# Optimization experiments

Hardware: AMD Instinct MI355X
Metric: run time of the kernel (lower is better)

The kernel has to match this reference:

```python
import jax, jax.numpy as jnp
import numpy as np

B, S, D, U = 32, 2048, 1024, 1024


def setup_inputs() -> dict:
    key = jax.random.key(0)
    ks = jax.random.split(key, 8)
    scale_in = 1.0 / np.sqrt(D)
    scale_u = 1.0 / np.sqrt(U)
    return {
        "query": jax.random.normal(ks[0], (B, D), dtype=jnp.float32),
        "values": jax.random.normal(ks[1], (B, S, D), dtype=jnp.float32),
        "W1": jax.random.normal(ks[2], (D, U), dtype=jnp.float32) * scale_in,
        "b1": jnp.zeros((U,), dtype=jnp.float32),
        "W2": jax.random.normal(ks[3], (D, U), dtype=jnp.float32) * scale_in,
        "b2": jnp.zeros((U,), dtype=jnp.float32),
        "V": jax.random.normal(ks[4], (U, 1), dtype=jnp.float32) * scale_u,
        "bV": jnp.zeros((1,), dtype=jnp.float32),
    }


def reference(query, values, W1, b1, W2, b2, V, bV):
    # values: [B, S, D] -> [B, S, U]; query: [B, D] -> [B, 1, U]
    proj_v = jnp.einsum("bsd,du->bsu", values, W1) + b1
    proj_q = (query @ W2 + b2)[:, None, :]
    # score: [B, S, 1]
    score = jnp.einsum("bsu,uo->bso", jnp.tanh(proj_v + proj_q), V) + bV
    attention_weights = jax.nn.softmax(score, axis=1)
    # context: [B, D]
    context_vector = jnp.sum(attention_weights * values, axis=1)
    return (context_vector, attention_weights)
```

## Files before the change

kernel.cpp:

```cpp
#include <hip/hip_runtime.h>

#define DEVFN __device__ __forceinline__
#define GLOBAL_AS __attribute__((address_space(1)))
#define LDS_AS __attribute__((address_space(3)))

typedef __attribute__((ext_vector_type(4))) float f32x4;
typedef __attribute__((ext_vector_type(8))) short short8;
typedef __attribute__((ext_vector_type(8))) unsigned short ushort8;

constexpr int CB = 32;
constexpr int CS = 2048;
constexpr int CD = 1024;
constexpr int CU = 1024;
constexpr int CM = CB * CS;

DEVFN unsigned f2bf_u(float f) {
    unsigned u = __float_as_uint(f);
    return (u + 0x7FFFu + ((u >> 16) & 1u)) >> 16;
}
DEVFN unsigned f2bf_pack(float lo, float hi) {
    return f2bf_u(lo) | (f2bf_u(hi) << 16);
}
DEVFN float tanh_fast(float x) {
    float e = exp2f(x * 2.885390081777927f);
    return 1.0f - 2.0f * __builtin_amdgcn_rcpf(e + 1.0f);
}

__global__ void k_bias1(const float* __restrict__ q, const float* __restrict__ W2,
                        float* __restrict__ bpart) {
    int dc = blockIdx.x, b = blockIdx.y;
    int t = threadIdx.x;
    __shared__ float qs[128];
    if (t < 128) qs[t] = q[b * CD + dc * 128 + t];
    __syncthreads();
    float acc0 = 0.f, acc1 = 0.f, acc2 = 0.f, acc3 = 0.f;
    const float* w2 = W2 + (size_t)(dc * 128) * CU + t;
#pragma unroll 4
    for (int d = 0; d < 128; ++d) {
        float qv = qs[d];
        const float* r = w2 + (size_t)d * CU;
        acc0 += qv * r[0];
        acc1 += qv * r[256];
        acc2 += qv * r[512];
        acc3 += qv * r[768];
    }
    float* o = bpart + (size_t)(b * 8 + dc) * CU + t;
    o[0] = acc0; o[256] = acc1; o[512] = acc2; o[768] = acc3;
}

__global__ void k_bias2(const float* __restrict__ bpart, const float* __restrict__ b1,
                        const float* __restrict__ b2, float* __restrict__ bias) {
    int idx = blockIdx.x * 256 + threadIdx.x;
    int b = idx >> 10, u = idx & 1023;
    float s = b1[u] + b2[u];
#pragma unroll
    for (int dc = 0; dc < 8; ++dc) s += bpart[(size_t)(b * 8 + dc) * CU + u];
    bias[idx] = s;
}

__global__ void k_packW1(const float* __restrict__ W1, unsigned short* __restrict__ W1p) {
    int tid = blockIdx.x * 256 + threadIdx.x;
    int o8  = tid * 8;
    int l   = (o8 >> 3) & 63;
    int ub  = (o8 >> 9) & 15;
    int ut  = (o8 >> 13) & 3;
    int kt  = o8 >> 15;
    int u  = ut * 256 + ub * 16 + (l & 15);
    int d0 = kt * 32 + (l >> 4) * 8;
    ushort8 v;
#pragma unroll
    for (int j = 0; j < 8; ++j)
        v[j] = (unsigned short)f2bf_u(W1[(size_t)(d0 + j) * CU + u]);
    *(ushort8*)(W1p + o8) = v;
}

__global__ __launch_bounds__(512, 2) void k_score(
    const float* __restrict__ values, const unsigned short* __restrict__ W1p,
    const float* __restrict__ bias, const float* __restrict__ V,
    float* __restrict__ score) {
    __shared__ __align__(16) char smem[8192];

    const int t = threadIdx.x;
    const int w = t >> 6, l = t & 63;
    const int m0 = blockIdx.x * 64;
    const int bb = m0 >> 11;

    const float* aSrcT = values + (size_t)(m0 + (t >> 3)) * CD + (t & 7) * 4;
    const int aWrByte = (t >> 7) * 1024
                      + (((t >> 3) & 15) | (((t >> 1) & 3) << 4)) * 16
                      + (t & 1) * 8;
    const unsigned short* bSrc = W1p + (size_t)w * 4096 + l * 8;

    f32x4 zero4 = {0.f, 0.f, 0.f, 0.f};
    f32x4 acc[4][8];
#pragma unroll
    for (int i = 0; i < 4; ++i)
#pragma unroll
        for (int j = 0; j < 8; ++j) acc[i][j] = zero4;

    short8 bFA[8], bFB[8];
    f32x4 aH0, aH1;

    {
#pragma unroll
        for (int jj = 0; jj < 8; ++jj)
            bFA[jj] = *(const short8*)(bSrc + jj * 512);
        aH0 = *(const f32x4*)(aSrcT);
        aH1 = *(const f32x4*)(aSrcT + 32);
        uint2 pk;
        pk.x = f2bf_pack(aH0[0], aH0[1]);
        pk.y = f2bf_pack(aH0[2], aH0[3]);
        *(uint2*)(smem + aWrByte) = pk;
        asm volatile("s_waitcnt lgkmcnt(0)" ::: "memory");
        asm volatile("s_barrier" ::: "memory");
    }

#define SCORE_BODY(KT, BF_CUR, BF_NXT, AH_LD, AH_WR, DO_LDB, DO_LDA, DO_WR)        \
    {                                                                               \
        if (DO_LDB) {                                                               \
            const unsigned short* bs = bSrc + (size_t)((KT) + 1) * 32768;           \
            _Pragma("unroll")                                                       \
            for (int jj = 0; jj < 8; ++jj)                                          \
                BF_NXT[jj] = *(const short8*)(bs + jj * 512);                       \
        }                                                                           \
        if (DO_LDA) AH_LD = *(const f32x4*)(aSrcT + ((KT) + 2) * 32);               \
        const char* aB = smem + ((KT) & 1) * 4096;                                  \
        short8 aF[4];                                                               \
        _Pragma("unroll")                                                           \
        for (int i = 0; i < 4; ++i)                                                 \
            aF[i] = *(const short8*)(aB + i * 1024 + l * 16);                       \
        __builtin_amdgcn_s_setprio(1);                                              \
        _Pragma("unroll")                                                           \
        for (int i = 0; i < 4; ++i)                                                 \
            _Pragma("unroll")                                                       \
            for (int j = 0; j < 8; ++j)                                             \
                acc[i][j] = __builtin_amdgcn_mfma_f32_16x16x32_bf16(                \
                    aF[i], BF_CUR[j], acc[i][j], 0, 0, 0);                          \
        __builtin_amdgcn_s_setprio(0);                                              \
        if (DO_WR) {                                                                \
            uint2 pk;                                                               \
            pk.x = f2bf_pack(AH_WR[0], AH_WR[1]);                                   \
            pk.y = f2bf_pack(AH_WR[2], AH_WR[3]);                                   \
            *(uint2*)(smem + (((KT) + 1) & 1) * 4096 + aWrByte) = pk;               \
        }                                                                           \
        asm volatile("s_waitcnt lgkmcnt(0)" ::: "memory");                          \
        asm volatile("s_barrier" ::: "memory");                                     \
    }

    for (int kt = 0; kt < 30; kt += 2) {
        SCORE_BODY(kt,     bFA, bFB, aH0, aH1, 1, 1, 1)
        SCORE_BODY(kt + 1, bFB, bFA, aH1, aH0, 1, 1, 1)
    }
    SCORE_BODY(30, bFA, bFB, aH0, aH1, 1, 0, 1)
    SCORE_BODY(31, bFB, bFA, aH1, aH0, 0, 0, 0)
#undef SCORE_BODY

    float part[4][4];
#pragma unroll
    for (int i = 0; i < 4; ++i)
#pragma unroll
        for (int rr = 0; rr < 4; ++rr) part[i][rr] = 0.f;

#pragma unroll
    for (int j = 0; j < 8; ++j) {
        int col = w * 128 + j * 16 + (l & 15);
        float vv = V[col];
        float bz = bias[bb * CU + col];
#pragma unroll
        for (int i = 0; i < 4; ++i)
#pragma unroll
            for (int rr = 0; rr < 4; ++rr)
                part[i][rr] += vv * tanh_fast(acc[i][j][rr] + bz);
    }

    __syncthreads();
    float* red = (float*)smem;
#pragma unroll
    for (int i = 0; i < 4; ++i)
#pragma unroll
        for (int rr = 0; rr < 4; ++rr) {
            float v = part[i][rr];
            v += __shfl_xor(v, 1);
            v += __shfl_xor(v, 2);
            v += __shfl_xor(v, 4);
            v += __shfl_xor(v, 8);
            if ((l & 15) == 0)
                red[w * 64 + i * 16 + (l >> 4) * 4 + rr] = v;
        }
    __syncthreads();
    if (t < 64) {
        float s = 0.f;
#pragma unroll
        for (int ww = 0; ww < 8; ++ww) s += red[ww * 64 + t];
        score[m0 + t] = s;
    }
}

__global__ void k_softmax(const float* __restrict__ score, float* __restrict__ wts) {
    int b = blockIdx.x, t = threadIdx.x;
    int i0 = b * CS + t, i1 = i0 + 1024;
    float s0 = score[i0];
    float s1 = score[i1];
    __shared__ float red[16];
    int wv = t >> 6, ln = t & 63;
    float m = fmaxf(s0, s1);
#pragma unroll
    for (int o = 32; o >= 1; o >>= 1) m = fmaxf(m, __shfl_xor(m, o));
    if (ln == 0) red[wv] = m;
    __syncthreads();
    float M = red[0];
#pragma unroll
    for (int k = 1; k < 16; ++k) M = fmaxf(M, red[k]);
    float e0 = __expf(s0 - M), e1 = __expf(s1 - M);
    float sm = e0 + e1;
#pragma unroll
    for (int o = 32; o >= 1; o >>= 1) sm += __shfl_xor(sm, o);
    __syncthreads();
    if (ln == 0) red[wv] = sm;
    __syncthreads();
    float T = 0.f;
#pragma unroll
    for (int k = 0; k < 16; ++k) T += red[k];
    float inv = 1.0f / T;
    wts[i0] = e0 * inv;
    wts[i1] = e1 * inv;
}

__global__ void k_ctx_part(const float* __restrict__ values, const float* __restrict__ wts,
                           float* __restrict__ part) {
    int b = blockIdx.y, sc = blockIdx.x;
    int t = threadIdx.x;
    const float* vb = values + ((size_t)b * CS + sc * 64) * CD + t * 4;
    const float* wb = wts + b * CS + sc * 64;
    f32x4 a = {0.f, 0.f, 0.f, 0.f};
#pragma unroll 8
    for (int s = 0; s < 64; ++s) {
        float wgt = wb[s];
        f32x4 v = *(const f32x4*)(vb + (size_t)s * CD);
        a += v * wgt;
    }
    *(f32x4*)(part + (size_t)(b * 32 + sc) * CD + t * 4) = a;
}

__global__ void k_ctx_red(const float* __restrict__ part, float* __restrict__ ctx) {
    int idx = blockIdx.x * 256 + threadIdx.x;
    int b = idx >> 10, d = idx & 1023;
    float s = 0.f;
#pragma unroll 8
    for (int c = 0; c < 32; ++c) s += part[(size_t)(b * 32 + c) * CD + d];
    ctx[idx] = s;
}

extern "C" void kernel_launch(void* const* d_in, const int* in_sizes, int n_in,
                              void* d_out, int out_size, void* d_ws, size_t ws_size,
                              hipStream_t stream) {
    const float* query  = (const float*)d_in[0];
    const float* values = (const float*)d_in[1];
    const float* W1     = (const float*)d_in[2];
    const float* b1     = (const float*)d_in[3];
    const float* W2     = (const float*)d_in[4];
    const float* b2     = (const float*)d_in[5];
    const float* V      = (const float*)d_in[6];

    float* out = (float*)d_out;
    float* ctx = out;
    float* wts = out + 32768;

    char* ws = (char*)d_ws;
    float*          score = (float*)ws;
    float*          bias  = (float*)(ws + (1 << 20));
    unsigned short* W1p   = (unsigned short*)(ws + (1 << 20) + (1 << 17));
    float*          part  = (float*)(ws + (1 << 20) + (1 << 17) + (1 << 21));
    float*          bpart = part;

    k_bias1<<<dim3(8, 32), 256, 0, stream>>>(query, W2, bpart);
    k_bias2<<<128, 256, 0, stream>>>(bpart, b1, b2, bias);
    k_packW1<<<512, 256, 0, stream>>>(W1, W1p);
    k_score<<<1024, 512, 0, stream>>>(values, W1p, bias, V, score);
    k_softmax<<<32, 1024, 0, stream>>>(score, wts);
    k_ctx_part<<<dim3(32, 32), 256, 0, stream>>>(values, wts, part);
    k_ctx_red<<<128, 256, 0, stream>>>(part, ctx);
}
```

Baseline: 235.8 us.

## Retile score GEMM to 128-row tiles split across two U halves with large LDS staging

The score GEMM now gives each block 128 rows of values and half of the U columns, instead of 64 rows and all of U. Each K-chunk of 256 columns of the A tile is staged as bf16 in a 128KB double-buffered, XOR-swizzled LDS area, so barriers drop from 32 to 4. Block IDs are remapped so that blocks sharing a row tile run together, which should let the second U half reuse the values rows from L2. Partial scores for the two U halves go to separate buffers and are summed in softmax. The cost is much higher LDS use per block, which limits occupancy, and each values row is now read by two blocks.

```diff
diff --git a/kernel.cpp b/kernel.cpp
--- a/kernel.cpp
+++ b/kernel.cpp
@@ -1,11 +1,10 @@
 #include <hip/hip_runtime.h>
 
 #define DEVFN __device__ __forceinline__
-#define GLOBAL_AS __attribute__((address_space(1)))
-#define LDS_AS __attribute__((address_space(3)))
 
 typedef __attribute__((ext_vector_type(4))) float f32x4;
 typedef __attribute__((ext_vector_type(8))) short short8;
+typedef __attribute__((ext_vector_type(4))) unsigned int uint4v;
 typedef __attribute__((ext_vector_type(8))) unsigned short ushort8;
 
 constexpr int CB = 32;
@@ -20,6 +19,14 @@
 }
 DEVFN unsigned f2bf_pack(float lo, float hi) {
     return f2bf_u(lo) | (f2bf_u(hi) << 16);
+}
+DEVFN short8 cvt8(f32x4 a, f32x4 b) {
+    uint4v p;
+    p[0] = f2bf_pack(a[0], a[1]);
+    p[1] = f2bf_pack(a[2], a[3]);
+    p[2] = f2bf_pack(b[0], b[1]);
+    p[3] = f2bf_pack(b[2], b[3]);
+    return __builtin_bit_cast(short8, p);
 }
 DEVFN float tanh_fast(float x) {
     float e = exp2f(x * 2.885390081777927f);
@@ -77,106 +84,127 @@
 __global__ __launch_bounds__(512, 2) void k_score(
     const float* __restrict__ values, const unsigned short* __restrict__ W1p,
     const float* __restrict__ bias, const float* __restrict__ V,
-    float* __restrict__ score) {
-    __shared__ __align__(16) char smem[8192];
+    float* __restrict__ score2) {
+    __shared__ __align__(16) char smem[131072];
 
     const int t = threadIdx.x;
     const int w = t >> 6, l = t & 63;
-    const int m0 = blockIdx.x * 64;
+    const int bid = blockIdx.x;
+    const int L = (bid >> 3) + (bid & 7) * 128;
+    const int xt = L >> 1, uc = L & 1;
+    const int m0 = xt * 128;
     const int bb = m0 >> 11;
 
-    const float* aSrcT = values + (size_t)(m0 + (t >> 3)) * CD + (t & 7) * 4;
-    const int aWrByte = (t >> 7) * 1024
-                      + (((t >> 3) & 15) | (((t >> 1) & 3) << 4)) * 16
-                      + (t & 1) * 8;
-    const unsigned short* bSrc = W1p + (size_t)w * 4096 + l * 8;
-
-    f32x4 zero4 = {0.f, 0.f, 0.f, 0.f};
-    f32x4 acc[4][8];
-#pragma unroll
-    for (int i = 0; i < 4; ++i)
-#pragma unroll
-        for (int j = 0; j < 8; ++j) acc[i][j] = zero4;
-
-    short8 bFA[8], bFB[8];
-    f32x4 aH0, aH1;
+    const float* sBase = values + (size_t)(m0 + (t >> 5)) * CD + (t & 31) * 8;
+    const int s2w = (t & 31) >> 2;
+    const int wrBase = s2w * 8192 + ((((t >> 5) + (t & 3) * 16)) ^ s2w) * 16;
+    const int lB = l * 16;
+    const unsigned short* bSrc = W1p + (size_t)(2 * uc + (w >> 2)) * 8192 + (w & 3) * 2048 + l * 8;
+
+    short8 bF0[4], bF1[4];
+    f32x4 stgA0, stgA1, stgB0, stgB1;
 
     {
-#pragma unroll
-        for (int jj = 0; jj < 8; ++jj)
-            bFA[jj] = *(const short8*)(bSrc + jj * 512);
-        aH0 = *(const f32x4*)(aSrcT);
-        aH1 = *(const f32x4*)(aSrcT + 32);
-        uint2 pk;
-        pk.x = f2bf_pack(aH0[0], aH0[1]);
-        pk.y = f2bf_pack(aH0[2], aH0[3]);
-        *(uint2*)(smem + aWrByte) = pk;
-        asm volatile("s_waitcnt lgkmcnt(0)" ::: "memory");
-        asm volatile("s_barrier" ::: "memory");
-    }
-
-#define SCORE_BODY(KT, BF_CUR, BF_NXT, AH_LD, AH_WR, DO_LDB, DO_LDA, DO_WR)        \
-    {                                                                               \
-        if (DO_LDB) {                                                               \
-            const unsigned short* bs = bSrc + (size_t)((KT) + 1) * 32768;           \
-            _Pragma("unroll")                                                       \
-            for (int jj = 0; jj < 8; ++jj)                                          \
-                BF_NXT[jj] = *(const short8*)(bs + jj * 512);                       \
-        }                                                                           \
-        if (DO_LDA) AH_LD = *(const f32x4*)(aSrcT + ((KT) + 2) * 32);               \
-        const char* aB = smem + ((KT) & 1) * 4096;                                  \
-        short8 aF[4];                                                               \
-        _Pragma("unroll")                                                           \
-        for (int i = 0; i < 4; ++i)                                                 \
-            aF[i] = *(const short8*)(aB + i * 1024 + l * 16);                       \
-        __builtin_amdgcn_s_setprio(1);                                              \
-        _Pragma("unroll")                                                           \
-        for (int i = 0; i < 4; ++i)                                                 \
-            _Pragma("unroll")                                                       \
-            for (int j = 0; j < 8; ++j)                                             \
-                acc[i][j] = __builtin_amdgcn_mfma_f32_16x16x32_bf16(                \
-                    aF[i], BF_CUR[j], acc[i][j], 0, 0, 0);                          \
-        __builtin_amdgcn_s_setprio(0);                                              \
-        if (DO_WR) {                                                                \
-            uint2 pk;                                                               \
-            pk.x = f2bf_pack(AH_WR[0], AH_WR[1]);                                   \
-            pk.y = f2bf_pack(AH_WR[2], AH_WR[3]);                                   \
-            *(uint2*)(smem + (((KT) + 1) & 1) * 4096 + aWrByte) = pk;               \
-        }                                                                           \
-        asm volatile("s_waitcnt lgkmcnt(0)" ::: "memory");                          \
-        asm volatile("s_barrier" ::: "memory");                                     \
-    }
-
-    for (int kt = 0; kt < 30; kt += 2) {
-        SCORE_BODY(kt,     bFA, bFB, aH0, aH1, 1, 1, 1)
-        SCORE_BODY(kt + 1, bFB, bFA, aH1, aH0, 1, 1, 1)
-    }
-    SCORE_BODY(30, bFA, bFB, aH0, aH1, 1, 0, 1)
-    SCORE_BODY(31, bFB, bFA, aH1, aH0, 0, 0, 0)
-#undef SCORE_BODY
-
-    float part[4][4];
-#pragma unroll
-    for (int i = 0; i < 4; ++i)
+        f32x4 pa[8], pb[8];
+#pragma unroll
+        for (int s = 0; s < 8; ++s) {
+            pa[s] = *(const f32x4*)(sBase + s * 16384);
+            pb[s] = *(const f32x4*)(sBase + s * 16384 + 4);
+        }
+#pragma unroll
+        for (int s = 0; s < 8; ++s)
+            *(short8*)(smem + wrBase + s * 1024) = cvt8(pa[s], pb[s]);
+    }
+#pragma unroll
+    for (int jj = 0; jj < 4; ++jj)
+        bF0[jj] = *(const short8*)(bSrc + jj * 512);
+    asm volatile("s_waitcnt lgkmcnt(0)" ::: "memory");
+    asm volatile("s_barrier" ::: "memory");
+
+    f32x4 acc[8][4];
+#pragma unroll
+    for (int i = 0; i < 8; ++i)
+#pragma unroll
+        for (int j = 0; j < 4; ++j) acc[i][j] = f32x4{0.f, 0.f, 0.f, 0.f};
+
+#pragma unroll
+    for (int cc = 0; cc < 4; ++cc) {
+        const int h = cc & 1;
+#pragma unroll
+        for (int s = 0; s < 8; ++s) {
+            const int kt = cc * 8 + s;
+            if (kt < 31) {
+                const unsigned short* bs = bSrc + (size_t)(kt + 1) * 32768;
+                if ((s & 1) == 0) {
+#pragma unroll
+                    for (int jj = 0; jj < 4; ++jj) bF1[jj] = *(const short8*)(bs + jj * 512);
+                } else {
+#pragma unroll
+                    for (int jj = 0; jj < 4; ++jj) bF0[jj] = *(const short8*)(bs + jj * 512);
+                }
+            }
+            short8 aF[8];
+#pragma unroll
+            for (int i = 0; i < 8; ++i)
+                aF[i] = *(const short8*)(smem + h * 65536 + s * 8192 + i * 1024 + (lB ^ (s * 16)));
+            if (cc < 3) {
+                if (s >= 2) {
+                    if ((s & 1) == 0)
+                        *(short8*)(smem + (h ^ 1) * 65536 + wrBase + (s - 2) * 1024) = cvt8(stgA0, stgA1);
+                    else
+                        *(short8*)(smem + (h ^ 1) * 65536 + wrBase + (s - 2) * 1024) = cvt8(stgB0, stgB1);
+                }
+                const float* sp = sBase + (cc + 1) * 256 + s * 16384;
+                if ((s & 1) == 0) { stgA0 = *(const f32x4*)sp; stgA1 = *(const f32x4*)(sp + 4); }
+                else              { stgB0 = *(const f32x4*)sp; stgB1 = *(const f32x4*)(sp + 4); }
+            }
+            __builtin_amdgcn_s_setprio(1);
+            if ((s & 1) == 0) {
+#pragma unroll
+                for (int j = 0; j < 4; ++j)
+#pragma unroll
+                    for (int i = 0; i < 8; ++i)
+                        acc[i][j] = __builtin_amdgcn_mfma_f32_16x16x32_bf16(
+                            aF[i], bF0[j], acc[i][j], 0, 0, 0);
+            } else {
+#pragma unroll
+                for (int j = 0; j < 4; ++j)
+#pragma unroll
+                    for (int i = 0; i < 8; ++i)
+                        acc[i][j] = __builtin_amdgcn_mfma_f32_16x16x32_bf16(
+                            aF[i], bF1[j], acc[i][j], 0, 0, 0);
+            }
+            __builtin_amdgcn_s_setprio(0);
+        }
+        if (cc < 3) {
+            *(short8*)(smem + ((cc & 1) ^ 1) * 65536 + wrBase + 6 * 1024) = cvt8(stgA0, stgA1);
+            *(short8*)(smem + ((cc & 1) ^ 1) * 65536 + wrBase + 7 * 1024) = cvt8(stgB0, stgB1);
+            asm volatile("s_waitcnt lgkmcnt(0)" ::: "memory");
+            asm volatile("s_barrier" ::: "memory");
+        }
+    }
+
+    float part[8][4];
+#pragma unroll
+    for (int i = 0; i < 8; ++i)
 #pragma unroll
         for (int rr = 0; rr < 4; ++rr) part[i][rr] = 0.f;
 
 #pragma unroll
-    for (int j = 0; j < 8; ++j) {
-        int col = w * 128 + j * 16 + (l & 15);
-        float vv = V[col];
-        float bz = bias[bb * CU + col];
-#pragma unroll
-        for (int i = 0; i < 4; ++i)
+    for (int j = 0; j < 4; ++j) {
+        const int col = uc * 512 + w * 64 + j * 16 + (l & 15);
+        const float vv = V[col];
+        const float bz = bias[bb * CU + col];
+#pragma unroll
+        for (int i = 0; i < 8; ++i)
 #pragma unroll
             for (int rr = 0; rr < 4; ++rr)
                 part[i][rr] += vv * tanh_fast(acc[i][j][rr] + bz);
     }
 
-    __syncthreads();
     float* red = (float*)smem;
 #pragma unroll
-    for (int i = 0; i < 4; ++i)
+    for (int i = 0; i < 8; ++i)
 #pragma unroll
         for (int rr = 0; rr < 4; ++rr) {
             float v = part[i][rr];
@@ -185,22 +213,22 @@
             v += __shfl_xor(v, 4);
             v += __shfl_xor(v, 8);
             if ((l & 15) == 0)
-                red[w * 64 + i * 16 + (l >> 4) * 4 + rr] = v;
+                red[w * 128 + i * 16 + (l >> 4) * 4 + rr] = v;
         }
     __syncthreads();
-    if (t < 64) {
-        float s = 0.f;
-#pragma unroll
-        for (int ww = 0; ww < 8; ++ww) s += red[ww * 64 + t];
-        score[m0 + t] = s;
-    }
-}
-
-__global__ void k_softmax(const float* __restrict__ score, float* __restrict__ wts) {
+    if (t < 128) {
+        float sv = 0.f;
+#pragma unroll
+        for (int ww = 0; ww < 8; ++ww) sv += red[ww * 128 + t];
+        score2[(size_t)uc * CM + m0 + t] = sv;
+    }
+}
+
+__global__ void k_softmax(const float* __restrict__ score2, float* __restrict__ wts) {
     int b = blockIdx.x, t = threadIdx.x;
     int i0 = b * CS + t, i1 = i0 + 1024;
-    float s0 = score[i0];
-    float s1 = score[i1];
+    float s0 = score2[i0] + score2[CM + i0];
+    float s1 = score2[i1] + score2[CM + i1];
     __shared__ float red[16];
     int wv = t >> 6, ln = t & 63;
     float m = fmaxf(s0, s1);
@@ -267,17 +295,17 @@
     float* wts = out + 32768;
 
     char* ws = (char*)d_ws;
-    float*          score = (float*)ws;
-    float*          bias  = (float*)(ws + (1 << 20));
-    unsigned short* W1p   = (unsigned short*)(ws + (1 << 20) + (1 << 17));
-    float*          part  = (float*)(ws + (1 << 20) + (1 << 17) + (1 << 21));
-    float*          bpart = part;
+    float*          score2 = (float*)ws;
+    float*          bias   = (float*)(ws + (1 << 20));
+    unsigned short* W1p    = (unsigned short*)(ws + (1 << 20) + (1 << 17));
+    float*          part   = (float*)(ws + (1 << 20) + (1 << 17) + (1 << 21));
+    float*          bpart  = part;
 
     k_bias1<<<dim3(8, 32), 256, 0, stream>>>(query, W2, bpart);
     k_bias2<<<128, 256, 0, stream>>>(bpart, b1, b2, bias);
     k_packW1<<<512, 256, 0, stream>>>(W1, W1p);
-    k_score<<<1024, 512, 0, stream>>>(values, W1p, bias, V, score);
-    k_softmax<<<32, 1024, 0, stream>>>(score, wts);
+    k_score<<<1024, 512, 0, stream>>>(values, W1p, bias, V, score2);
+    k_softmax<<<32, 1024, 0, stream>>>(score2, wts);
     k_ctx_part<<<dim3(32, 32), 256, 0, stream>>>(values, wts, part);
     k_ctx_red<<<128, 256, 0, stream>>>(part, ctx);
 }
```

Measured after the change: 386.7 us. +64.0%, slower.
